# Kernel tuning notes

Hardware: AMD Instinct MI355X
Metric: run time of the kernel (lower is better)

The kernel has to match this reference:

```python
import jax, jax.numpy as jnp
import numpy as np
import math

D_MODEL = 1024
NHEAD = 16
HEAD_DIM = D_MODEL // NHEAD
SCALE = math.sqrt(HEAD_DIM)
B, TQ, TK = 8, 1024, 1024


def setup_inputs() -> dict:
    key = jax.random.key(0)
    ks = jax.random.split(key, 8)
    init = 0.02
    return {
        "query": jax.random.normal(ks[0], (B, TQ, D_MODEL), jnp.float32),
        "memory": jax.random.normal(ks[1], (B, TK, D_MODEL), jnp.float32),
        "coverage": jax.random.uniform(ks[2], (B, TK), jnp.float32),
        "Wq": jax.random.normal(ks[3], (D_MODEL, D_MODEL), jnp.float32) * init,
        "bq": jnp.zeros((D_MODEL,), jnp.float32),
        "Wk": jax.random.normal(ks[4], (D_MODEL, D_MODEL), jnp.float32) * init,
        "bk": jnp.zeros((D_MODEL,), jnp.float32),
        "Wv": jax.random.normal(ks[5], (D_MODEL, D_MODEL), jnp.float32) * init,
        "bv": jnp.zeros((D_MODEL,), jnp.float32),
        "Wo": jax.random.normal(ks[6], (D_MODEL, D_MODEL), jnp.float32) * init,
        "bo": jnp.zeros((D_MODEL,), jnp.float32),
        "Wcov": jax.random.normal(ks[7], (NHEAD, 1), jnp.float32) * init,
    }


def reference(query, memory, coverage, Wq, bq, Wk, bk, Wv, bv, Wo, bo, Wcov):
    b, tq, _ = query.shape
    tk = memory.shape[1]
    # projections, split into heads: [B, H, T, hd]
    Q = (query @ Wq.T + bq).reshape(b, tq, NHEAD, HEAD_DIM).transpose(0, 2, 1, 3)
    K = (memory @ Wk.T + bk).reshape(b, tk, NHEAD, HEAD_DIM).transpose(0, 2, 1, 3)
    V = (memory @ Wv.T + bv).reshape(b, tk, NHEAD, HEAD_DIM).transpose(0, 2, 1, 3)
    scores = jnp.einsum('bhqd,bhkd->bhqk', Q, K) / SCALE
    # coverage_proj: Linear(1, nhead, bias=False) -> outer product coverage x Wcov[:,0]
    cov_bias = jnp.einsum('bk,h->bhk', coverage, Wcov[:, 0])[:, :, None, :]  # [B,H,1,Tk]
    scores = scores + cov_bias
    attn = jax.nn.softmax(scores, axis=-1)
    # dropout is identity in eval/deterministic mode
    out = jnp.einsum('bhqk,bhkd->bhqd', attn, V).transpose(0, 2, 1, 3).reshape(b, tq, D_MODEL)
    out = out @ Wo.T + bo
    new_coverage = coverage + attn.mean(axis=1).sum(axis=1)  # [B,Tk]
    return out, new_coverage
```

## Files before the change

kernel.cpp:

```cpp
#include <hip/hip_runtime.h>

typedef __bf16 bf16_t;
typedef bf16_t bf16x8 __attribute__((ext_vector_type(8)));
typedef float f32x4 __attribute__((ext_vector_type(4)));

#define MFMA16(a, b, c) __builtin_amdgcn_mfma_f32_16x16x32_bf16(a, b, c, 0, 0, 0)

#define LOG2E 1.44269504f
#define C1 0.18033688f

__device__ inline void async_copy16(const bf16_t* g, bf16_t* l) {
  __builtin_amdgcn_global_load_lds(
      (const __attribute__((address_space(1))) void*)g,
      (__attribute__((address_space(3))) void*)l, 16, 0, 0);
}

__device__ inline bf16x8 lds_frag(const bf16_t* lds, int row, int c8) {
  return *(const bf16x8*)(lds + row * 64 + ((c8 ^ (row & 7)) << 3));
}

template <int NCHUNK>
__device__ inline void stage_tile(const bf16_t* __restrict__ g, size_t ld,
                                  bf16_t* lds, int tid) {
#pragma unroll
  for (int it = 0; it < NCHUNK / 256; ++it) {
    int f = it * 256 + tid;
    int row = f >> 3;
    int c8 = (f & 7) ^ (row & 7);
    async_copy16(g + (size_t)row * ld + c8 * 8, lds + f * 8);
  }
}

__global__ __launch_bounds__(256) void convert_kernel(
    const float* __restrict__ q, const float* __restrict__ mem,
    const float* __restrict__ wq, const float* __restrict__ wk,
    const float* __restrict__ wv, const float* __restrict__ wo,
    const float* __restrict__ coverage, bf16_t* Xq, bf16_t* Xm, bf16_t* Wqb,
    bf16_t* Wkb, bf16_t* Wvb, bf16_t* Wob, float* covout) {
  size_t i = ((size_t)blockIdx.x * 256 + threadIdx.x) * 8;
  if (i >= 20971520u) {
    size_t off = i - 20971520u;
    *(float4*)(covout + off) = *(const float4*)(coverage + off);
    *(float4*)(covout + off + 4) = *(const float4*)(coverage + off + 4);
    return;
  }
  const float* src;
  bf16_t* dst;
  size_t off;
  if (i < 8388608u)        { src = q;   dst = Xq;  off = i; }
  else if (i < 16777216u)  { src = mem; dst = Xm;  off = i - 8388608u; }
  else if (i < 17825792u)  { src = wq;  dst = Wqb; off = i - 16777216u; }
  else if (i < 18874368u)  { src = wk;  dst = Wkb; off = i - 17825792u; }
  else if (i < 19922944u)  { src = wv;  dst = Wvb; off = i - 18874368u; }
  else                     { src = wo;  dst = Wob; off = i - 19922944u; }
  float4 f0 = *(const float4*)(src + off);
  float4 f1 = *(const float4*)(src + off + 4);
  union { bf16_t h[8]; uint4 u; } t;
  t.h[0] = (bf16_t)f0.x; t.h[1] = (bf16_t)f0.y;
  t.h[2] = (bf16_t)f0.z; t.h[3] = (bf16_t)f0.w;
  t.h[4] = (bf16_t)f1.x; t.h[5] = (bf16_t)f1.y;
  t.h[6] = (bf16_t)f1.z; t.h[7] = (bf16_t)f1.w;
  *(uint4*)(dst + off) = t.u;
}

template <int MODE>
__global__ __launch_bounds__(256) void gemm_nt(
    const bf16_t* __restrict__ A, const bf16_t* __restrict__ Bw,
    const float* __restrict__ bias, void* __restrict__ Cout) {
  __shared__ bf16_t As[128 * 64];
  __shared__ bf16_t Bs[128 * 64];
  const int tid = threadIdx.x;
  const int wave = tid >> 6, lane = tid & 63, quad = lane >> 4, c = lane & 15;
  const int wm = (wave & 1) * 64, wn = (wave >> 1) * 64;
  const size_t bm = blockIdx.x, bn = blockIdx.y;
  const bf16_t* Ab = A + bm * 128 * 1024;
  const bf16_t* Bb = Bw + bn * 128 * 1024;
  const f32x4 z4 = {0.f, 0.f, 0.f, 0.f};
  f32x4 acc[4][4];
#pragma unroll
  for (int i = 0; i < 4; ++i)
#pragma unroll
    for (int j = 0; j < 4; ++j) acc[i][j] = z4;

  for (int kt = 0; kt < 16; ++kt) {
    if (kt) __syncthreads();
    stage_tile<1024>(Ab + kt * 64, 1024, As, tid);
    stage_tile<1024>(Bb + kt * 64, 1024, Bs, tid);
    __syncthreads();
#pragma unroll
    for (int ks = 0; ks < 2; ++ks) {
      bf16x8 af[4], bfr[4];
#pragma unroll
      for (int i = 0; i < 4; ++i)
        af[i] = lds_frag(As, wm + 16 * i + c, ks * 4 + quad);
#pragma unroll
      for (int j = 0; j < 4; ++j)
        bfr[j] = lds_frag(Bs, wn + 16 * j + c, ks * 4 + quad);
#pragma unroll
      for (int i = 0; i < 4; ++i)
#pragma unroll
        for (int j = 0; j < 4; ++j)
          acc[i][j] = MFMA16(af[i], bfr[j], acc[i][j]);
    }
  }
#pragma unroll
  for (int i = 0; i < 4; ++i)
#pragma unroll
    for (int j = 0; j < 4; ++j) {
      int gc = (int)bn * 128 + wn + 16 * j + c;
      float bvv = bias[gc];
      if (MODE == 2) {
        int b = (int)(bm >> 3);
        int kk = (int)(bm & 7) * 128 + wm + 16 * i + quad * 4;
        union { bf16_t h4[4]; uint2 u; } pk;
#pragma unroll
        for (int r = 0; r < 4; ++r) pk.h4[r] = (bf16_t)(acc[i][j][r] + bvv);
        *(uint2*)((bf16_t*)Cout + ((size_t)(b * 1024 + gc)) * 1024 + kk) = pk.u;
      } else {
        int gr0 = (int)bm * 128 + wm + 16 * i + quad * 4;
#pragma unroll
        for (int r = 0; r < 4; ++r) {
          float v = acc[i][j][r] + bvv;
          size_t idx = (size_t)(gr0 + r) * 1024 + gc;
          if (MODE == 1)
            ((float*)Cout)[idx] = v;
          else
            ((bf16_t*)Cout)[idx] = (bf16_t)v;
        }
      }
    }
}

__global__ __launch_bounds__(256) void attn_fwd(
    const bf16_t* __restrict__ Qp, const bf16_t* __restrict__ Kp,
    const bf16_t* __restrict__ Vt, const float* __restrict__ coverage,
    const float* __restrict__ Wcov, bf16_t* __restrict__ Hb,
    float* __restrict__ linvG) {
  __shared__ bf16_t Qs[64 * 64];
  __shared__ bf16_t Ks[64 * 64];
  __shared__ bf16_t Vs[64 * 64];
  __shared__ bf16_t Ps[4][16 * 64];
  __shared__ float covb[1024];
  const int tid = threadIdx.x;
  const int wave = tid >> 6, lane = tid & 63, quad = lane >> 4, c = lane & 15;
  const int q0 = blockIdx.x * 64, h = blockIdx.y, b = blockIdx.z;
  const float wcl = Wcov[h] * LOG2E;
  const f32x4 z4 = {0.f, 0.f, 0.f, 0.f};

  stage_tile<512>(Qp + ((size_t)(b * 1024 + q0)) * 1024 + h * 64, 1024, Qs,
                  tid);
  for (int i = tid; i < 1024; i += 256) covb[i] = coverage[b * 1024 + i] * wcl;

  float lpart = 0.f;
  f32x4 O[4] = {z4, z4, z4, z4};
  bf16x8 qf0, qf1;
  bf16_t* Pw = &Ps[wave][0];

  for (int kt = 0; kt < 16; ++kt) {
    const int k0 = kt * 64;
    if (kt) __syncthreads();
    stage_tile<512>(Kp + ((size_t)(b * 1024 + k0)) * 1024 + h * 64, 1024, Ks,
                    tid);
    stage_tile<512>(Vt + ((size_t)(b * 1024 + h * 64)) * 1024 + k0, 1024, Vs,
                    tid);
    __syncthreads();
    if (kt == 0) {
      qf0 = lds_frag(Qs, wave * 16 + c, quad);
      qf1 = lds_frag(Qs, wave * 16 + c, 4 + quad);
    }
    f32x4 S[4] = {z4, z4, z4, z4};
#pragma unroll
    for (int j = 0; j < 4; ++j) {
      S[j] = MFMA16(lds_frag(Ks, j * 16 + c, quad), qf0, S[j]);
      S[j] = MFMA16(lds_frag(Ks, j * 16 + c, 4 + quad), qf1, S[j]);
    }
#pragma unroll
    for (int j = 0; j < 4; ++j) {
      f32x4 cb = *(const f32x4*)&covb[k0 + j * 16 + quad * 4];
      union { bf16_t h4[4]; uint2 u; } pk;
#pragma unroll
      for (int r = 0; r < 4; ++r) {
        float p = exp2f(S[j][r] * C1 + cb[r]);
        lpart += p;
        pk.h4[r] = (bf16_t)p;
      }
      int k8 = j * 2 + (quad >> 1);
      *(uint2*)(Pw + c * 64 + ((k8 ^ (c & 7)) << 3) + (quad & 1) * 4) = pk.u;
    }
#pragma unroll
    for (int ks = 0; ks < 2; ++ks) {
      bf16x8 pb = *(const bf16x8*)(Pw + c * 64 + (((ks * 4 + quad) ^ (c & 7)) << 3));
#pragma unroll
      for (int j = 0; j < 4; ++j)
        O[j] = MFMA16(lds_frag(Vs, j * 16 + c, ks * 4 + quad), pb, O[j]);
    }
  }

  lpart += __shfl_xor(lpart, 16);
  lpart += __shfl_xor(lpart, 32);
  float linv = 1.f / lpart;
  if (quad == 0)
    linvG[((size_t)(b * 16 + h)) * 1024 + q0 + wave * 16 + c] = linv;

  size_t rowbase = ((size_t)(b * 1024 + q0 + wave * 16 + c)) * 1024 + h * 64;
#pragma unroll
  for (int j = 0; j < 4; ++j) {
    union { bf16_t h4[4]; uint2 u; } pk;
#pragma unroll
    for (int r = 0; r < 4; ++r) pk.h4[r] = (bf16_t)(O[j][r] * linv);
    *(uint2*)(Hb + rowbase + j * 16 + quad * 4) = pk.u;
  }
}

__global__ __launch_bounds__(256) void cov_kernel(
    const bf16_t* __restrict__ Qp, const bf16_t* __restrict__ Kp,
    const float* __restrict__ coverage, const float* __restrict__ Wcov,
    const float* __restrict__ linvG, float* __restrict__ covout) {
  __shared__ bf16_t Ks[64 * 64];
  __shared__ bf16_t Qs[64 * 64];
  __shared__ float covb[64];
  __shared__ float covsum[64];
  const int tid = threadIdx.x;
  const int wave = tid >> 6, lane = tid & 63, quad = lane >> 4, c = lane & 15;
  const int k0 = blockIdx.x * 64, h = blockIdx.y, b = blockIdx.z;
  const float wcl = Wcov[h] * LOG2E;
  const f32x4 z4 = {0.f, 0.f, 0.f, 0.f};

  stage_tile<512>(Kp + ((size_t)(b * 1024 + k0)) * 1024 + h * 64, 1024, Ks,
                  tid);
  if (tid < 64) {
    covb[tid] = coverage[b * 1024 + k0 + tid] * wcl;
    covsum[tid] = 0.f;
  }
  float cs[4][4] = {};
  bf16x8 kf0[4], kf1[4];

  for (int qt = 0; qt < 16; ++qt) {
    if (qt) __syncthreads();
    stage_tile<512>(Qp + ((size_t)(b * 1024 + qt * 64)) * 1024 + h * 64, 1024,
                    Qs, tid);
    float lv = linvG[((size_t)(b * 16 + h)) * 1024 + qt * 64 + wave * 16 + c];
    __syncthreads();
    if (qt == 0) {
#pragma unroll
      for (int j = 0; j < 4; ++j) {
        kf0[j] = lds_frag(Ks, j * 16 + c, quad);
        kf1[j] = lds_frag(Ks, j * 16 + c, 4 + quad);
      }
    }
    bf16x8 qf0 = lds_frag(Qs, wave * 16 + c, quad);
    bf16x8 qf1 = lds_frag(Qs, wave * 16 + c, 4 + quad);
    f32x4 S[4] = {z4, z4, z4, z4};
#pragma unroll
    for (int j = 0; j < 4; ++j) {
      S[j] = MFMA16(kf0[j], qf0, S[j]);
      S[j] = MFMA16(kf1[j], qf1, S[j]);
    }
#pragma unroll
    for (int j = 0; j < 4; ++j) {
      f32x4 cb = *(const f32x4*)&covb[j * 16 + quad * 4];
#pragma unroll
      for (int r = 0; r < 4; ++r)
        cs[j][r] += exp2f(S[j][r] * C1 + cb[r]) * lv;
    }
  }
#pragma unroll
  for (int j = 0; j < 4; ++j)
#pragma unroll
    for (int r = 0; r < 4; ++r) {
      float v = cs[j][r];
      v += __shfl_xor(v, 1);
      v += __shfl_xor(v, 2);
      v += __shfl_xor(v, 4);
      v += __shfl_xor(v, 8);
      if (c == 0) atomicAdd(&covsum[j * 16 + quad * 4 + r], v);
    }
  __syncthreads();
  if (tid < 64)
    atomicAdd(&covout[b * 1024 + k0 + tid], covsum[tid] * 0.0625f);
}

extern "C" void kernel_launch(void* const* d_in, const int* in_sizes, int n_in,
                              void* d_out, int out_size, void* d_ws,
                              size_t ws_size, hipStream_t stream) {
  const float* query = (const float*)d_in[0];
  const float* memory = (const float*)d_in[1];
  const float* coverage = (const float*)d_in[2];
  const float* Wq = (const float*)d_in[3];
  const float* bq = (const float*)d_in[4];
  const float* Wk = (const float*)d_in[5];
  const float* bk = (const float*)d_in[6];
  const float* Wv = (const float*)d_in[7];
  const float* bv = (const float*)d_in[8];
  const float* Wo = (const float*)d_in[9];
  const float* bo = (const float*)d_in[10];
  const float* Wcov = (const float*)d_in[11];

  char* w = (char*)d_ws;
  const size_t MB = 1024 * 1024;
  bf16_t* Xq = (bf16_t*)(w + 0);
  bf16_t* Xm = (bf16_t*)(w + 16 * MB);
  bf16_t* Wqb = (bf16_t*)(w + 32 * MB);
  bf16_t* Wkb = (bf16_t*)(w + 34 * MB);
  bf16_t* Wvb = (bf16_t*)(w + 36 * MB);
  bf16_t* Wob = (bf16_t*)(w + 38 * MB);
  bf16_t* Qp = (bf16_t*)(w + 40 * MB);
  bf16_t* Kp = (bf16_t*)(w + 56 * MB);
  bf16_t* Vt = (bf16_t*)(w + 72 * MB);
  bf16_t* Hb = (bf16_t*)(w + 0);
  float* linvG = (float*)(w + 16 * MB);

  float* out = (float*)d_out;
  float* covout = out + (size_t)8 * 1024 * 1024;

  convert_kernel<<<10244, 256, 0, stream>>>(query, memory, Wq, Wk, Wv, Wo,
                                            coverage, Xq, Xm, Wqb, Wkb, Wvb,
                                            Wob, covout);
  gemm_nt<0><<<dim3(64, 8), 256, 0, stream>>>(Xq, Wqb, bq, Qp);
  gemm_nt<0><<<dim3(64, 8), 256, 0, stream>>>(Xm, Wkb, bk, Kp);
  gemm_nt<2><<<dim3(64, 8), 256, 0, stream>>>(Xm, Wvb, bv, Vt);
  attn_fwd<<<dim3(16, 16, 8), 256, 0, stream>>>(Qp, Kp, Vt, coverage, Wcov,
                                                Hb, linvG);
  gemm_nt<1><<<dim3(64, 8), 256, 0, stream>>>(Hb, Wob, bo, out);
  cov_kernel<<<dim3(16, 16, 8), 256, 0, stream>>>(Qp, Kp, coverage, Wcov,
                                                  linvG, covout);
}
```

Measured before the change: 348.4 us.

## Fuse coverage accumulation into attention kernel with deterministic partial reduce

Each attention block now handles 128 queries with 512 threads. After the PV pass it makes a second sweep over K tiles, recomputing the scores and adding up the normalized probabilities per key into shared memory. The per-block partials go to a workspace buffer and a small reduce kernel combines them with the old coverage. This removes the separate cov_kernel, its global atomics and the linvG round trip, and it drops the coverage copy from the convert kernel. The cost is a second QK pass inside the attention kernel and larger blocks, which may lower occupancy.

```diff
diff --git a/kernel.cpp b/kernel.cpp
--- a/kernel.cpp
+++ b/kernel.cpp
@@ -19,12 +19,12 @@
   return *(const bf16x8*)(lds + row * 64 + ((c8 ^ (row & 7)) << 3));
 }
 
-template <int NCHUNK>
+template <int NCHUNK, int NT>
 __device__ inline void stage_tile(const bf16_t* __restrict__ g, size_t ld,
                                   bf16_t* lds, int tid) {
 #pragma unroll
-  for (int it = 0; it < NCHUNK / 256; ++it) {
-    int f = it * 256 + tid;
+  for (int it = 0; it < NCHUNK / NT; ++it) {
+    int f = it * NT + tid;
     int row = f >> 3;
     int c8 = (f & 7) ^ (row & 7);
     async_copy16(g + (size_t)row * ld + c8 * 8, lds + f * 8);
@@ -34,16 +34,9 @@
 __global__ __launch_bounds__(256) void convert_kernel(
     const float* __restrict__ q, const float* __restrict__ mem,
     const float* __restrict__ wq, const float* __restrict__ wk,
-    const float* __restrict__ wv, const float* __restrict__ wo,
-    const float* __restrict__ coverage, bf16_t* Xq, bf16_t* Xm, bf16_t* Wqb,
-    bf16_t* Wkb, bf16_t* Wvb, bf16_t* Wob, float* covout) {
+    const float* __restrict__ wv, const float* __restrict__ wo, bf16_t* Xq,
+    bf16_t* Xm, bf16_t* Wqb, bf16_t* Wkb, bf16_t* Wvb, bf16_t* Wob) {
   size_t i = ((size_t)blockIdx.x * 256 + threadIdx.x) * 8;
-  if (i >= 20971520u) {
-    size_t off = i - 20971520u;
-    *(float4*)(covout + off) = *(const float4*)(coverage + off);
-    *(float4*)(covout + off + 4) = *(const float4*)(coverage + off + 4);
-    return;
-  }
   const float* src;
   bf16_t* dst;
   size_t off;
@@ -84,8 +77,8 @@
 
   for (int kt = 0; kt < 16; ++kt) {
     if (kt) __syncthreads();
-    stage_tile<1024>(Ab + kt * 64, 1024, As, tid);
-    stage_tile<1024>(Bb + kt * 64, 1024, Bs, tid);
+    stage_tile<1024, 256>(Ab + kt * 64, 1024, As, tid);
+    stage_tile<1024, 256>(Bb + kt * 64, 1024, Bs, tid);
     __syncthreads();
 #pragma unroll
     for (int ks = 0; ks < 2; ++ks) {
@@ -131,25 +124,30 @@
     }
 }
 
-__global__ __launch_bounds__(256) void attn_fwd(
+__global__ __launch_bounds__(512) void attn_fwd(
     const bf16_t* __restrict__ Qp, const bf16_t* __restrict__ Kp,
     const bf16_t* __restrict__ Vt, const float* __restrict__ coverage,
     const float* __restrict__ Wcov, bf16_t* __restrict__ Hb,
-    float* __restrict__ linvG) {
-  __shared__ bf16_t Qs[64 * 64];
+    float* __restrict__ part) {
+  __shared__ bf16_t Qs[128 * 64];
   __shared__ bf16_t Ks[64 * 64];
   __shared__ bf16_t Vs[64 * 64];
-  __shared__ bf16_t Ps[4][16 * 64];
+  __shared__ bf16_t Ps[8][16 * 64];
   __shared__ float covb[1024];
+  __shared__ float covsum[1024];
   const int tid = threadIdx.x;
   const int wave = tid >> 6, lane = tid & 63, quad = lane >> 4, c = lane & 15;
-  const int q0 = blockIdx.x * 64, h = blockIdx.y, b = blockIdx.z;
+  const int qx = blockIdx.x, h = blockIdx.y, b = blockIdx.z;
+  const int q0 = qx * 128;
   const float wcl = Wcov[h] * LOG2E;
   const f32x4 z4 = {0.f, 0.f, 0.f, 0.f};
 
-  stage_tile<512>(Qp + ((size_t)(b * 1024 + q0)) * 1024 + h * 64, 1024, Qs,
-                  tid);
-  for (int i = tid; i < 1024; i += 256) covb[i] = coverage[b * 1024 + i] * wcl;
+  stage_tile<1024, 512>(Qp + ((size_t)(b * 1024 + q0)) * 1024 + h * 64, 1024,
+                        Qs, tid);
+  for (int i = tid; i < 1024; i += 512) {
+    covb[i] = coverage[b * 1024 + i] * wcl;
+    covsum[i] = 0.f;
+  }
 
   float lpart = 0.f;
   f32x4 O[4] = {z4, z4, z4, z4};
@@ -159,10 +157,10 @@
   for (int kt = 0; kt < 16; ++kt) {
     const int k0 = kt * 64;
     if (kt) __syncthreads();
-    stage_tile<512>(Kp + ((size_t)(b * 1024 + k0)) * 1024 + h * 64, 1024, Ks,
-                    tid);
-    stage_tile<512>(Vt + ((size_t)(b * 1024 + h * 64)) * 1024 + k0, 1024, Vs,
-                    tid);
+    stage_tile<512, 512>(Kp + ((size_t)(b * 1024 + k0)) * 1024 + h * 64, 1024,
+                         Ks, tid);
+    stage_tile<512, 512>(Vt + ((size_t)(b * 1024 + h * 64)) * 1024 + k0, 1024,
+                         Vs, tid);
     __syncthreads();
     if (kt == 0) {
       qf0 = lds_frag(Qs, wave * 16 + c, quad);
@@ -189,7 +187,8 @@
     }
 #pragma unroll
     for (int ks = 0; ks < 2; ++ks) {
-      bf16x8 pb = *(const bf16x8*)(Pw + c * 64 + (((ks * 4 + quad) ^ (c & 7)) << 3));
+      bf16x8 pb =
+          *(const bf16x8*)(Pw + c * 64 + (((ks * 4 + quad) ^ (c & 7)) << 3));
 #pragma unroll
       for (int j = 0; j < 4; ++j)
         O[j] = MFMA16(lds_frag(Vs, j * 16 + c, ks * 4 + quad), pb, O[j]);
@@ -199,8 +198,6 @@
   lpart += __shfl_xor(lpart, 16);
   lpart += __shfl_xor(lpart, 32);
   float linv = 1.f / lpart;
-  if (quad == 0)
-    linvG[((size_t)(b * 16 + h)) * 1024 + q0 + wave * 16 + c] = linv;
 
   size_t rowbase = ((size_t)(b * 1024 + q0 + wave * 16 + c)) * 1024 + h * 64;
 #pragma unroll
@@ -210,74 +207,49 @@
     for (int r = 0; r < 4; ++r) pk.h4[r] = (bf16_t)(O[j][r] * linv);
     *(uint2*)(Hb + rowbase + j * 16 + quad * 4) = pk.u;
   }
-}
-
-__global__ __launch_bounds__(256) void cov_kernel(
-    const bf16_t* __restrict__ Qp, const bf16_t* __restrict__ Kp,
-    const float* __restrict__ coverage, const float* __restrict__ Wcov,
-    const float* __restrict__ linvG, float* __restrict__ covout) {
-  __shared__ bf16_t Ks[64 * 64];
-  __shared__ bf16_t Qs[64 * 64];
-  __shared__ float covb[64];
-  __shared__ float covsum[64];
-  const int tid = threadIdx.x;
-  const int wave = tid >> 6, lane = tid & 63, quad = lane >> 4, c = lane & 15;
-  const int k0 = blockIdx.x * 64, h = blockIdx.y, b = blockIdx.z;
-  const float wcl = Wcov[h] * LOG2E;
-  const f32x4 z4 = {0.f, 0.f, 0.f, 0.f};
-
-  stage_tile<512>(Kp + ((size_t)(b * 1024 + k0)) * 1024 + h * 64, 1024, Ks,
-                  tid);
-  if (tid < 64) {
-    covb[tid] = coverage[b * 1024 + k0 + tid] * wcl;
-    covsum[tid] = 0.f;
-  }
-  float cs[4][4] = {};
-  bf16x8 kf0[4], kf1[4];
-
-  for (int qt = 0; qt < 16; ++qt) {
-    if (qt) __syncthreads();
-    stage_tile<512>(Qp + ((size_t)(b * 1024 + qt * 64)) * 1024 + h * 64, 1024,
-                    Qs, tid);
-    float lv = linvG[((size_t)(b * 16 + h)) * 1024 + qt * 64 + wave * 16 + c];
-    __syncthreads();
-    if (qt == 0) {
-#pragma unroll
-      for (int j = 0; j < 4; ++j) {
-        kf0[j] = lds_frag(Ks, j * 16 + c, quad);
-        kf1[j] = lds_frag(Ks, j * 16 + c, 4 + quad);
-      }
-    }
-    bf16x8 qf0 = lds_frag(Qs, wave * 16 + c, quad);
-    bf16x8 qf1 = lds_frag(Qs, wave * 16 + c, 4 + quad);
+
+  float linv_r[4];
+#pragma unroll
+  for (int r = 0; r < 4; ++r) linv_r[r] = __shfl(linv, quad * 4 + r);
+
+  for (int kt = 0; kt < 16; ++kt) {
+    const int k0 = kt * 64;
+    __syncthreads();
+    stage_tile<512, 512>(Kp + ((size_t)(b * 1024 + k0)) * 1024 + h * 64, 1024,
+                         Ks, tid);
+    __syncthreads();
     f32x4 S[4] = {z4, z4, z4, z4};
 #pragma unroll
     for (int j = 0; j < 4; ++j) {
-      S[j] = MFMA16(kf0[j], qf0, S[j]);
-      S[j] = MFMA16(kf1[j], qf1, S[j]);
-    }
-#pragma unroll
-    for (int j = 0; j < 4; ++j) {
-      f32x4 cb = *(const f32x4*)&covb[j * 16 + quad * 4];
+      S[j] = MFMA16(qf0, lds_frag(Ks, j * 16 + c, quad), S[j]);
+      S[j] = MFMA16(qf1, lds_frag(Ks, j * 16 + c, 4 + quad), S[j]);
+    }
+#pragma unroll
+    for (int j = 0; j < 4; ++j) {
+      float cb = covb[k0 + j * 16 + c];
+      float vsum = 0.f;
 #pragma unroll
       for (int r = 0; r < 4; ++r)
-        cs[j][r] += exp2f(S[j][r] * C1 + cb[r]) * lv;
-    }
-  }
-#pragma unroll
-  for (int j = 0; j < 4; ++j)
-#pragma unroll
-    for (int r = 0; r < 4; ++r) {
-      float v = cs[j][r];
-      v += __shfl_xor(v, 1);
-      v += __shfl_xor(v, 2);
-      v += __shfl_xor(v, 4);
-      v += __shfl_xor(v, 8);
-      if (c == 0) atomicAdd(&covsum[j * 16 + quad * 4 + r], v);
-    }
+        vsum += exp2f(S[j][r] * C1 + cb) * linv_r[r];
+      vsum += __shfl_xor(vsum, 16);
+      vsum += __shfl_xor(vsum, 32);
+      if (quad == 0) atomicAdd(&covsum[k0 + j * 16 + c], vsum);
+    }
+  }
   __syncthreads();
-  if (tid < 64)
-    atomicAdd(&covout[b * 1024 + k0 + tid], covsum[tid] * 0.0625f);
+  float* ps = part + ((size_t)(b * 128 + h * 8 + qx)) * 1024;
+  for (int i = tid; i < 1024; i += 512) ps[i] = covsum[i];
+}
+
+__global__ __launch_bounds__(256) void cov_reduce(
+    const float* __restrict__ part, const float* __restrict__ coverage,
+    float* __restrict__ covout) {
+  int i = blockIdx.x * 256 + threadIdx.x;
+  int b = i >> 10, k = i & 1023;
+  const float* p = part + (size_t)b * 128 * 1024 + k;
+  float s = 0.f;
+  for (int j = 0; j < 128; ++j) s += p[(size_t)j * 1024];
+  covout[i] = coverage[i] + s * 0.0625f;
 }
 
 extern "C" void kernel_launch(void* const* d_in, const int* in_sizes, int n_in,
@@ -308,20 +280,18 @@
   bf16_t* Kp = (bf16_t*)(w + 56 * MB);
   bf16_t* Vt = (bf16_t*)(w + 72 * MB);
   bf16_t* Hb = (bf16_t*)(w + 0);
-  float* linvG = (float*)(w + 16 * MB);
+  float* part = (float*)(w + 16 * MB);
 
   float* out = (float*)d_out;
   float* covout = out + (size_t)8 * 1024 * 1024;
 
-  convert_kernel<<<10244, 256, 0, stream>>>(query, memory, Wq, Wk, Wv, Wo,
-                                            coverage, Xq, Xm, Wqb, Wkb, Wvb,
-                                            Wob, covout);
+  convert_kernel<<<10240, 256, 0, stream>>>(query, memory, Wq, Wk, Wv, Wo, Xq,
+                                            Xm, Wqb, Wkb, Wvb, Wob);
   gemm_nt<0><<<dim3(64, 8), 256, 0, stream>>>(Xq, Wqb, bq, Qp);
   gemm_nt<0><<<dim3(64, 8), 256, 0, stream>>>(Xm, Wkb, bk, Kp);
   gemm_nt<2><<<dim3(64, 8), 256, 0, stream>>>(Xm, Wvb, bv, Vt);
-  attn_fwd<<<dim3(16, 16, 8), 256, 0, stream>>>(Qp, Kp, Vt, coverage, Wcov,
-                                                Hb, linvG);
+  attn_fwd<<<dim3(8, 16, 8), 512, 0, stream>>>(Qp, Kp, Vt, coverage, Wcov, Hb,
+                                               part);
   gemm_nt<1><<<dim3(64, 8), 256, 0, stream>>>(Hb, Wob, bo, out);
-  cov_kernel<<<dim3(16, 16, 8), 256, 0, stream>>>(Qp, Kp, coverage, Wcov,
-                                                  linvG, covout);
-}
+  cov_reduce<<<32, 256, 0, stream>>>(part, coverage, covout);
+}
```

After: 360.3 us. 1.03x slower.
